# Kernel tuning notes

Measured on AMD Instinct MI355X. Metric: run time of the kernel, lower is better.

## Reference

```python
import jax, jax.numpy as jnp
import numpy as np


def setup_inputs() -> dict:
    key = jax.random.key(0)
    kq, kk, kv = jax.random.split(key, 3)
    n, d = 8192, 32
    return {
        "Q": jax.random.normal(kq, (n, d), dtype=jnp.float32),
        "K": jax.random.normal(kk, (n, d), dtype=jnp.float32),
        "V": jax.random.normal(kv, (n, d), dtype=jnp.float32),
    }


def reference(Q, K, V):
    # FlashAttention-2 tiling with online softmax is mathematically equivalent
    # to full (unscaled, unmasked) softmax attention: O = softmax(Q K^T) V.
    # Note: the original module applies NO 1/sqrt(d) scaling.
    S = jnp.einsum("qd,kd->qk", Q, K)           # [n, n]
    P = jax.nn.softmax(S, axis=-1)                # numerically stable softmax
    return jnp.einsum("qk,kd->qd", P, V)         # [n, d]
```

## Files before the change

kernel.cpp:

```cpp
#include <hip/hip_runtime.h>
#include <hip/hip_bf16.h>

typedef __bf16 bf16x8 __attribute__((ext_vector_type(8)));
typedef __bf16 bf16x4 __attribute__((ext_vector_type(4)));
typedef float  f32x4  __attribute__((ext_vector_type(4)));
typedef unsigned short u16;

static constexpr int N = 8192;
static constexpr int D = 32;
static constexpr float L2E = 1.44269504088896340736f;
static constexpr float MSHIFT = 32.0f;

__device__ __forceinline__ void gl_lds16(const u16* g, u16* l) {
  __builtin_amdgcn_global_load_lds(
      (const __attribute__((address_space(1))) unsigned int*)g,
      (__attribute__((address_space(3))) unsigned int*)l, 16, 0, 0);
}

__global__ __launch_bounds__(256) void prep_kernel(
    const float* __restrict__ Q, const float* __restrict__ K,
    const float* __restrict__ V, u16* __restrict__ Qb, u16* __restrict__ Kb,
    u16* __restrict__ Vt) {
  __shared__ float tile[64][33];
  const int b = blockIdx.x;
  auto pack = [](float x, float y) -> unsigned int {
    u16 ux = __builtin_bit_cast(u16, (__bf16)x);
    u16 uy = __builtin_bit_cast(u16, (__bf16)y);
    return (unsigned int)ux | ((unsigned int)uy << 16);
  };
  if (b < 256) {
    const int i = (b * 256 + threadIdx.x) * 4;
    const float4 q = *reinterpret_cast<const float4*>(Q + i);
    const float4 k = *reinterpret_cast<const float4*>(K + i);
    uint2 qo = { pack(q.x * L2E, q.y * L2E), pack(q.z * L2E, q.w * L2E) };
    uint2 ko = { pack(k.x, k.y), pack(k.z, k.w) };
    *reinterpret_cast<uint2*>(Qb + i) = qo;
    *reinterpret_cast<uint2*>(Kb + i) = ko;
  } else {
    const int r0 = (b - 256) * 64;
    const int row = threadIdx.x >> 2;
    const int c0 = (threadIdx.x & 3) * 8;
    const float4 x0 = *reinterpret_cast<const float4*>(V + (size_t)(r0 + row) * D + c0);
    const float4 x1 = *reinterpret_cast<const float4*>(V + (size_t)(r0 + row) * D + c0 + 4);
    tile[row][c0 + 0] = x0.x; tile[row][c0 + 1] = x0.y;
    tile[row][c0 + 2] = x0.z; tile[row][c0 + 3] = x0.w;
    tile[row][c0 + 4] = x1.x; tile[row][c0 + 5] = x1.y;
    tile[row][c0 + 6] = x1.z; tile[row][c0 + 7] = x1.w;
    __syncthreads();
    const int d = threadIdx.x >> 3;
    const int kc = (threadIdx.x & 7) * 8;
    uint4 o;
    o.x = pack(tile[kc + 0][d], tile[kc + 1][d]);
    o.y = pack(tile[kc + 2][d], tile[kc + 3][d]);
    o.z = pack(tile[kc + 4][d], tile[kc + 5][d]);
    o.w = pack(tile[kc + 6][d], tile[kc + 7][d]);
    *reinterpret_cast<uint4*>(Vt + (size_t)d * N + r0 + kc) = o;
  }
}

template <int NS>
__global__ __launch_bounds__(256, 4) void flash_kernel(
    const u16* __restrict__ Qb, const u16* __restrict__ Kb,
    const u16* __restrict__ Vt, float* __restrict__ lP,
    float* __restrict__ OP) {
  constexpr int KPB = N / NS;
  constexpr int NT = KPB / 64;
  __shared__ u16 Ks[2][2048];
  __shared__ u16 Vs[2][2048];

  const int tid = threadIdx.x;
  const int lane = tid & 63;
  const int wave = tid >> 6;
  const int a = lane & 15;
  const int g = lane >> 4;
  const int qg = blockIdx.x & 63;
  const int sp = blockIdx.x >> 6;
  const int qr0 = qg * 128 + wave * 32;
  const int k0 = sp * KPB;

  const bf16x8 qfA = *reinterpret_cast<const bf16x8*>(Qb + (qr0 + a) * D + g * 8);
  const bf16x8 qfB = *reinterpret_cast<const bf16x8*>(Qb + (qr0 + 16 + a) * D + g * 8);

  const int krow = tid >> 2;
  const int kslot = (tid & 3) ^ ((krow >> 1) & 3);
  const u16* __restrict__ ksrc = Kb + krow * D + kslot * 8;
  const int vd = tid >> 3;
  const int vlb = (tid & 7) ^ (vd & 7);
  const u16* __restrict__ vsrc = Vt + (size_t)vd * N + vlb * 8;
  u16* const kdst = &Ks[0][0] + wave * 512;
  u16* const vdst = &Vs[0][0] + wave * 512;

  const f32x4 minit = {-MSHIFT, -MSHIFT, -MSHIFT, -MSHIFT};
  const f32x4 zero4 = {0.f, 0.f, 0.f, 0.f};
  f32x4 accA0 = zero4, accA1 = zero4, accB0 = zero4, accB1 = zero4;
  float lA = 0.f, lB = 0.f;

  gl_lds16(ksrc + (size_t)k0 * D, kdst);
  gl_lds16(vsrc + k0, vdst);
  __syncthreads();

#pragma unroll
  for (int t = 0; t < NT; ++t) {
    const int cur = t & 1;
    if (t + 1 < NT) {
      const int kb = k0 + (t + 1) * 64;
      gl_lds16(ksrc + (size_t)kb * D, kdst + (cur ^ 1) * 2048);
      gl_lds16(vsrc + kb, vdst + (cur ^ 1) * 2048);
    }
    __builtin_amdgcn_sched_barrier(0);

    bf16x8 kf[4];
#pragma unroll
    for (int t4 = 0; t4 < 4; ++t4) {
      const int row = 16 * t4 + a;
      kf[t4] = *reinterpret_cast<const bf16x8*>(
          &Ks[cur][row * 32 + ((g ^ ((a >> 1) & 3)) << 3)]);
    }
    bf16x4 v0[4], v1[4];
#pragma unroll
    for (int tt = 0; tt < 4; ++tt) {
      const int pb = ((tt << 1) + (g >> 1)) ^ (a & 7);
      const int off = pb * 8 + (g & 1) * 4;
      v0[tt] = *reinterpret_cast<const bf16x4*>(&Vs[cur][a * 64 + off]);
      v1[tt] = *reinterpret_cast<const bf16x4*>(&Vs[cur][(16 + a) * 64 + off]);
    }

    f32x4 sA[4], sB[4];
#pragma unroll
    for (int t4 = 0; t4 < 4; ++t4) {
      sA[t4] = __builtin_amdgcn_mfma_f32_16x16x32_bf16(kf[t4], qfA, minit, 0, 0, 0);
      sB[t4] = __builtin_amdgcn_mfma_f32_16x16x32_bf16(kf[t4], qfB, minit, 0, 0, 0);
    }

    float pA[4][4], pB[4][4];
    float psA = 0.f, psB = 0.f;
#pragma unroll
    for (int t4 = 0; t4 < 4; ++t4) {
      float sa = 0.f, sb = 0.f;
#pragma unroll
      for (int r = 0; r < 4; ++r) {
        pA[t4][r] = __builtin_amdgcn_exp2f(sA[t4][r]);
        pB[t4][r] = __builtin_amdgcn_exp2f(sB[t4][r]);
        sa += pA[t4][r];
        sb += pB[t4][r];
      }
      psA += sa;
      psB += sb;
    }
    lA += psA;
    lB += psB;

    const bf16x8 pfA0 = {(__bf16)pA[0][0], (__bf16)pA[0][1], (__bf16)pA[0][2], (__bf16)pA[0][3],
                         (__bf16)pA[1][0], (__bf16)pA[1][1], (__bf16)pA[1][2], (__bf16)pA[1][3]};
    const bf16x8 pfA1 = {(__bf16)pA[2][0], (__bf16)pA[2][1], (__bf16)pA[2][2], (__bf16)pA[2][3],
                         (__bf16)pA[3][0], (__bf16)pA[3][1], (__bf16)pA[3][2], (__bf16)pA[3][3]};
    const bf16x8 pfB0 = {(__bf16)pB[0][0], (__bf16)pB[0][1], (__bf16)pB[0][2], (__bf16)pB[0][3],
                         (__bf16)pB[1][0], (__bf16)pB[1][1], (__bf16)pB[1][2], (__bf16)pB[1][3]};
    const bf16x8 pfB1 = {(__bf16)pB[2][0], (__bf16)pB[2][1], (__bf16)pB[2][2], (__bf16)pB[2][3],
                         (__bf16)pB[3][0], (__bf16)pB[3][1], (__bf16)pB[3][2], (__bf16)pB[3][3]};

    const bf16x8 va00 = __builtin_shufflevector(v0[0], v0[1], 0, 1, 2, 3, 4, 5, 6, 7);
    const bf16x8 va01 = __builtin_shufflevector(v0[2], v0[3], 0, 1, 2, 3, 4, 5, 6, 7);
    const bf16x8 va10 = __builtin_shufflevector(v1[0], v1[1], 0, 1, 2, 3, 4, 5, 6, 7);
    const bf16x8 va11 = __builtin_shufflevector(v1[2], v1[3], 0, 1, 2, 3, 4, 5, 6, 7);

    accA0 = __builtin_amdgcn_mfma_f32_16x16x32_bf16(va00, pfA0, accA0, 0, 0, 0);
    accA1 = __builtin_amdgcn_mfma_f32_16x16x32_bf16(va10, pfA0, accA1, 0, 0, 0);
    accB0 = __builtin_amdgcn_mfma_f32_16x16x32_bf16(va00, pfB0, accB0, 0, 0, 0);
    accB1 = __builtin_amdgcn_mfma_f32_16x16x32_bf16(va10, pfB0, accB1, 0, 0, 0);
    accA0 = __builtin_amdgcn_mfma_f32_16x16x32_bf16(va01, pfA1, accA0, 0, 0, 0);
    accA1 = __builtin_amdgcn_mfma_f32_16x16x32_bf16(va11, pfA1, accA1, 0, 0, 0);
    accB0 = __builtin_amdgcn_mfma_f32_16x16x32_bf16(va01, pfB1, accB0, 0, 0, 0);
    accB1 = __builtin_amdgcn_mfma_f32_16x16x32_bf16(va11, pfB1, accB1, 0, 0, 0);

    __syncthreads();
  }

  lA += __shfl_xor(lA, 16, 64);
  lA += __shfl_xor(lA, 32, 64);
  lB += __shfl_xor(lB, 16, 64);
  lB += __shfl_xor(lB, 32, 64);

  float* obA = OP + (size_t)(sp * N + qr0 + a) * D;
  float* obB = OP + (size_t)(sp * N + qr0 + 16 + a) * D;
#pragma unroll
  for (int r = 0; r < 4; ++r) {
    obA[4 * g + r] = accA0[r];
    obA[16 + 4 * g + r] = accA1[r];
    obB[4 * g + r] = accB0[r];
    obB[16 + 4 * g + r] = accB1[r];
  }
  if (g == 0) {
    lP[sp * N + qr0 + a] = lA;
    lP[sp * N + qr0 + 16 + a] = lB;
  }
}

template <int NS>
__global__ __launch_bounds__(256) void combine_kernel(
    const float* __restrict__ lP, const float* __restrict__ OP,
    float* __restrict__ out) {
  const int idx = blockIdx.x * 256 + threadIdx.x;
  if (idx >= N * D) return;
  const int q = idx >> 5;
  float L = 0.f, o = 0.f;
#pragma unroll
  for (int s = 0; s < NS; ++s) {
    L += lP[s * N + q];
    o += OP[(size_t)s * N * D + idx];
  }
  out[idx] = o / L;
}

extern "C" void kernel_launch(void* const* d_in, const int* in_sizes, int n_in,
                              void* d_out, int out_size, void* d_ws, size_t ws_size,
                              hipStream_t stream) {
  const float* Q = (const float*)d_in[0];
  const float* K = (const float*)d_in[1];
  const float* V = (const float*)d_in[2];
  float* out = (float*)d_out;

  const size_t base = (size_t)3 * N * D * sizeof(u16);
  const size_t per_split = (size_t)N * sizeof(float) + (size_t)N * D * sizeof(float);
  int ns = 16;
  while (ns > 4 && base + (size_t)ns * per_split > ws_size) ns >>= 1;

  u16* Qb = (u16*)d_ws;
  u16* Kb = Qb + N * D;
  u16* Vt = Kb + N * D;
  float* lP = (float*)(Vt + N * D);
  float* OP = lP + ns * N;

  prep_kernel<<<256 + N / 64, 256, 0, stream>>>(Q, K, V, Qb, Kb, Vt);
  switch (ns) {
    case 16:
      flash_kernel<16><<<64 * 16, 256, 0, stream>>>(Qb, Kb, Vt, lP, OP);
      combine_kernel<16><<<(N * D) / 256, 256, 0, stream>>>(lP, OP, out);
      break;
    case 8:
      flash_kernel<8><<<64 * 8, 256, 0, stream>>>(Qb, Kb, Vt, lP, OP);
      combine_kernel<8><<<(N * D) / 256, 256, 0, stream>>>(lP, OP, out);
      break;
    default:
      flash_kernel<4><<<64 * 4, 256, 0, stream>>>(Qb, Kb, Vt, lP, OP);
      combine_kernel<4><<<(N * D) / 256, 256, 0, stream>>>(lP, OP, out);
      break;
  }
}
```

Before: 33.91 us.

## Fuse split-K combine into flash kernel via last-block atomic counter

Removes the separate combine kernel launch: each flash block publishes its partial output and row sums, increments a per-query-group atomic counter, and the last block to finish for that group performs the reduction and writes the final output. Partial output stores are also vectorized to f32x4. This removes one kernel launch and its associated gap, at the cost of atomics and fences plus a serialized tail reduction done by the last block of each group. The counters are reset inside the prep kernel.

```diff
diff --git a/kernel.cpp b/kernel.cpp
--- a/kernel.cpp
+++ b/kernel.cpp
@@ -20,9 +20,10 @@
 __global__ __launch_bounds__(256) void prep_kernel(
     const float* __restrict__ Q, const float* __restrict__ K,
     const float* __restrict__ V, u16* __restrict__ Qb, u16* __restrict__ Kb,
-    u16* __restrict__ Vt) {
+    u16* __restrict__ Vt, int* __restrict__ cnt) {
   __shared__ float tile[64][33];
   const int b = blockIdx.x;
+  if (b == 0 && threadIdx.x < 64) cnt[threadIdx.x] = 0;
   auto pack = [](float x, float y) -> unsigned int {
     u16 ux = __builtin_bit_cast(u16, (__bf16)x);
     u16 uy = __builtin_bit_cast(u16, (__bf16)y);
@@ -62,11 +63,12 @@
 __global__ __launch_bounds__(256, 4) void flash_kernel(
     const u16* __restrict__ Qb, const u16* __restrict__ Kb,
     const u16* __restrict__ Vt, float* __restrict__ lP,
-    float* __restrict__ OP) {
+    float* __restrict__ OP, float* __restrict__ out, int* __restrict__ cnt) {
   constexpr int KPB = N / NS;
   constexpr int NT = KPB / 64;
   __shared__ u16 Ks[2][2048];
   __shared__ u16 Vs[2][2048];
+  __shared__ int last_flag;
 
   const int tid = threadIdx.x;
   const int lane = tid & 63;
@@ -183,33 +185,41 @@
 
   float* obA = OP + (size_t)(sp * N + qr0 + a) * D;
   float* obB = OP + (size_t)(sp * N + qr0 + 16 + a) * D;
-#pragma unroll
-  for (int r = 0; r < 4; ++r) {
-    obA[4 * g + r] = accA0[r];
-    obA[16 + 4 * g + r] = accA1[r];
-    obB[4 * g + r] = accB0[r];
-    obB[16 + 4 * g + r] = accB1[r];
-  }
+  *reinterpret_cast<f32x4*>(obA + 4 * g) = accA0;
+  *reinterpret_cast<f32x4*>(obA + 16 + 4 * g) = accA1;
+  *reinterpret_cast<f32x4*>(obB + 4 * g) = accB0;
+  *reinterpret_cast<f32x4*>(obB + 16 + 4 * g) = accB1;
   if (g == 0) {
     lP[sp * N + qr0 + a] = lA;
     lP[sp * N + qr0 + 16 + a] = lB;
   }
-}
-
-template <int NS>
-__global__ __launch_bounds__(256) void combine_kernel(
-    const float* __restrict__ lP, const float* __restrict__ OP,
-    float* __restrict__ out) {
-  const int idx = blockIdx.x * 256 + threadIdx.x;
-  if (idx >= N * D) return;
-  const int q = idx >> 5;
-  float L = 0.f, o = 0.f;
-#pragma unroll
-  for (int s = 0; s < NS; ++s) {
-    L += lP[s * N + q];
-    o += OP[(size_t)s * N * D + idx];
-  }
-  out[idx] = o / L;
+
+  __syncthreads();
+  if (tid == 0) {
+    __threadfence();
+    const int v = __hip_atomic_fetch_add(&cnt[qg], 1, __ATOMIC_ACQ_REL,
+                                         __HIP_MEMORY_SCOPE_AGENT);
+    last_flag = (v == NS - 1);
+  }
+  __syncthreads();
+  if (last_flag) {
+    __threadfence();
+#pragma unroll
+    for (int k = 0; k < 4; ++k) {
+      const int i4 = k * 256 + tid;
+      const int q = qg * 128 + (i4 >> 3);
+      const int db = i4 & 7;
+      float L = 0.f;
+      f32x4 o = {0.f, 0.f, 0.f, 0.f};
+#pragma unroll
+      for (int s = 0; s < NS; ++s) {
+        L += lP[s * N + q];
+        o += *reinterpret_cast<const f32x4*>(OP + ((size_t)s * N + q) * D + db * 4);
+      }
+      const float inv = 1.0f / L;
+      *reinterpret_cast<f32x4*>(out + (size_t)q * D + db * 4) = o * inv;
+    }
+  }
 }
 
 extern "C" void kernel_launch(void* const* d_in, const int* in_sizes, int n_in,
@@ -223,27 +233,20 @@
   const size_t base = (size_t)3 * N * D * sizeof(u16);
   const size_t per_split = (size_t)N * sizeof(float) + (size_t)N * D * sizeof(float);
   int ns = 16;
-  while (ns > 4 && base + (size_t)ns * per_split > ws_size) ns >>= 1;
+  while (ns > 4 && base + (size_t)ns * per_split + 256 > ws_size) ns >>= 1;
 
   u16* Qb = (u16*)d_ws;
   u16* Kb = Qb + N * D;
   u16* Vt = Kb + N * D;
   float* lP = (float*)(Vt + N * D);
   float* OP = lP + ns * N;
-
-  prep_kernel<<<256 + N / 64, 256, 0, stream>>>(Q, K, V, Qb, Kb, Vt);
-  switch (ns) {
-    case 16:
-      flash_kernel<16><<<64 * 16, 256, 0, stream>>>(Qb, Kb, Vt, lP, OP);
-      combine_kernel<16><<<(N * D) / 256, 256, 0, stream>>>(lP, OP, out);
-      break;
-    case 8:
-      flash_kernel<8><<<64 * 8, 256, 0, stream>>>(Qb, Kb, Vt, lP, OP);
-      combine_kernel<8><<<(N * D) / 256, 256, 0, stream>>>(lP, OP, out);
-      break;
-    default:
-      flash_kernel<4><<<64 * 4, 256, 0, stream>>>(Qb, Kb, Vt, lP, OP);
-      combine_kernel<4><<<(N * D) / 256, 256, 0, stream>>>(lP, OP, out);
-      break;
-  }
-}
+  int* cnt = (int*)(OP + (size_t)ns * N * D);
+
+  prep_kernel<<<256 + N / 64, 256, 0, stream>>>(Q, K, V, Qb, Kb, Vt, cnt);
+  if (ns == 16)
+    flash_kernel<16><<<64 * 16, 256, 0, stream>>>(Qb, Kb, Vt, lP, OP, out, cnt);
+  else if (ns == 8)
+    flash_kernel<8><<<64 * 8, 256, 0, stream>>>(Qb, Kb, Vt, lP, OP, out, cnt);
+  else
+    flash_kernel<4><<<64 * 4, 256, 0, stream>>>(Qb, Kb, Vt, lP, OP, out, cnt);
+}
```

Result: slower. 85.37 us (+151.8%).
